# Optimization experiments

Hardware: AMD Instinct MI355X
Metric: run time of the kernel (lower is better)

Reference implementation:

```python
import jax, jax.numpy as jnp
import numpy as np

N_NODES = 100000
N_EDGES = 50000
NNZ = 800000
C = 256
EPS = 0.0  # fixed (train_eps=False)


def setup_inputs() -> dict:
    key = jax.random.key(0)
    k1, k2, k3, k4, k5 = jax.random.split(key, 5)
    x_0 = jax.random.normal(k1, (N_NODES, C), dtype=jnp.float32)
    node_idx = jax.random.randint(k2, (NNZ,), 0, N_NODES, dtype=jnp.int64 if jax.config.jax_enable_x64 else jnp.int32)
    edge_idx = jax.random.randint(k3, (NNZ,), 0, N_EDGES, dtype=jnp.int64 if jax.config.jax_enable_x64 else jnp.int32)
    W = jax.random.normal(k4, (C, C), dtype=jnp.float32) / np.sqrt(C)
    b = jax.random.normal(k5, (C,), dtype=jnp.float32) * 0.01
    return {"x_0": x_0, "node_idx": node_idx, "edge_idx": edge_idx, "W": W, "b": b}


def reference(x_0, node_idx, edge_idx, W, b):
    # vertex2edge: x_1 = B_1^T @ x_0  (each hyperedge sums its member nodes)
    x_1 = jax.ops.segment_sum(x_0[node_idx], edge_idx, num_segments=N_EDGES)  # (E, C)
    # edge2vertex: m_{1->0} = B_1 @ x_1  (each node sums its incident hyperedges)
    m_1_0 = jax.ops.segment_sum(x_1[edge_idx], node_idx, num_segments=N_NODES)  # (N, C)
    # GIN update: Theta @ ((1+eps) x_0 + m)
    x_0_out = ((1.0 + EPS) * x_0 + m_1_0) @ W.T + b
    # use_norm=False -> no row normalization
    return (x_0_out, x_1)
```

## Files before the change

kernel.cpp:

```cpp
#include <hip/hip_runtime.h>

#define N_NODES 100000
#define N_EDGES 50000
#define NNZ     800000
#define C       256

#define SHC_E 8
#define SHC_N 9
#define NBC_E ((N_EDGES + (1 << SHC_E) - 1) >> SHC_E)
#define NBC_N ((N_NODES + (1 << SHC_N) - 1) >> SHC_N)
#define CHUNK 4096
#define NCHUNK ((NNZ + CHUNK - 1) / CHUNK)

#define CONV_BLOCKS (N_NODES * C / 4 / 256)
#define PREPW_BLOCKS 32

typedef short  bf16x8 __attribute__((ext_vector_type(8)));
typedef float  f32x4  __attribute__((ext_vector_type(4)));

static __device__ __forceinline__ unsigned short f2bf(float f) {
    unsigned int u = __float_as_uint(f);
    u += 0x7FFF + ((u >> 16) & 1);
    return (unsigned short)(u >> 16);
}
static __device__ __forceinline__ float bf2f(unsigned short u) {
    return __uint_as_float(((unsigned int)u) << 16);
}


__global__ void convert_hist(const float* __restrict__ x0, unsigned short* __restrict__ x0b,
                             const int* __restrict__ node_idx, const int* __restrict__ edge_idx,
                             int* __restrict__ gcnt_e, int* __restrict__ gcnt_n,
                             int* __restrict__ chunkhist_e, int* __restrict__ chunkhist_n,
                             const float* __restrict__ W, unsigned short* __restrict__ Wb) {
    int bid = blockIdx.x;
    if (bid < CONV_BLOCKS) {
        size_t i = (size_t)bid * 256 + threadIdx.x;
        float4 v = ((const float4*)x0)[i];
        ushort4 o;
        o.x = f2bf(v.x); o.y = f2bf(v.y); o.z = f2bf(v.z); o.w = f2bf(v.w);
        ((ushort4*)x0b)[i] = o;
    } else if (bid < CONV_BLOCKS + NCHUNK) {
        __shared__ int he[NBC_E], hn[NBC_N];
        const int tid = threadIdx.x;
        const int chunk = bid - CONV_BLOCKS;
        for (int i = tid; i < NBC_E; i += 256) he[i] = 0;
        for (int i = tid; i < NBC_N; i += 256) hn[i] = 0;
        __syncthreads();
        const int start = chunk * CHUNK;
        const int end = (start + CHUNK < NNZ) ? start + CHUNK : NNZ;
        for (int k = start + tid; k < end; k += 256) {
            atomicAdd(&he[edge_idx[k] >> SHC_E], 1);
            atomicAdd(&hn[node_idx[k] >> SHC_N], 1);
        }
        __syncthreads();
        for (int i = tid; i < NBC_E; i += 256) {
            int c = he[i];
            chunkhist_e[chunk * NBC_E + i] = c;
            if (c) atomicAdd(&gcnt_e[i], c);
        }
        for (int i = tid; i < NBC_N; i += 256) {
            int c = hn[i];
            chunkhist_n[chunk * NBC_N + i] = c;
            if (c) atomicAdd(&gcnt_n[i], c);
        }
    } else {
        int idx = (bid - CONV_BLOCKS - NCHUNK) * 256 + threadIdx.x;
        int h = idx >> 12, i = idx & 4095;
        int t = i >> 9, s = (i >> 6) & 7, l = i & 63;
        int m = l & 15, q = l >> 4;
        const float* src = W + (size_t)(h * 128 + 16 * t + m) * C + 32 * s + 8 * q;
        float4 f0 = *(const float4*)(src);
        float4 f1 = *(const float4*)(src + 4);
        unsigned short* d = Wb + (size_t)idx * 8;
        d[0] = f2bf(f0.x); d[1] = f2bf(f0.y); d[2] = f2bf(f0.z); d[3] = f2bf(f0.w);
        d[4] = f2bf(f1.x); d[5] = f2bf(f1.y); d[6] = f2bf(f1.z); d[7] = f2bf(f1.w);
    }
}


__global__ void coarse_scan(const int* __restrict__ gcnt_e, const int* __restrict__ gcnt_n,
                            int* __restrict__ gbase_e, int* __restrict__ gbase_n,
                            int* __restrict__ gcur_e, int* __restrict__ gcur_n) {
    const int* gcnt = (blockIdx.x == 0) ? gcnt_e : gcnt_n;
    int* gbase = (blockIdx.x == 0) ? gbase_e : gbase_n;
    int* gcur  = (blockIdx.x == 0) ? gcur_e : gcur_n;
    const int nb = (blockIdx.x == 0) ? NBC_E : NBC_N;
    int tid = threadIdx.x, lane = tid & 63, wid = tid >> 6;
    int v = (tid < nb) ? gcnt[tid] : 0;
    int incl = v;
#pragma unroll
    for (int s = 1; s < 64; s <<= 1) { int u = __shfl_up(incl, s, 64); if (lane >= s) incl += u; }
    __shared__ int wsum[4];
    if (lane == 63) wsum[wid] = incl;
    __syncthreads();
    int add = 0;
    for (int i = 0; i < wid; i++) add += wsum[i];
    int excl = add + incl - v;
    if (tid <= nb) gbase[tid] = excl;
    if (tid < nb)  gcur[tid]  = excl;
}


__global__ __launch_bounds__(256) void bin_coarse(const int* __restrict__ node_idx,
                                                  const int* __restrict__ edge_idx,
                                                  int* __restrict__ gcur_e, int* __restrict__ gcur_n,
                                                  const int* __restrict__ chunkhist_e,
                                                  const int* __restrict__ chunkhist_n,
                                                  unsigned int* __restrict__ tmp_e,
                                                  unsigned int* __restrict__ tmp_n) {
    __shared__ int hist_e[NBC_E], hist_n[NBC_N];
    __shared__ int base_e[NBC_E], base_n[NBC_N];
    const int tid = threadIdx.x;
    const int chunk = blockIdx.x;
    const int start = chunk * CHUNK;
    const int end = (start + CHUNK < NNZ) ? start + CHUNK : NNZ;

    for (int i = tid; i < NBC_E; i += 256) {
        int c = chunkhist_e[chunk * NBC_E + i];
        base_e[i] = c ? atomicAdd(&gcur_e[i], c) : 0;
        hist_e[i] = 0;
    }
    for (int i = tid; i < NBC_N; i += 256) {
        int c = chunkhist_n[chunk * NBC_N + i];
        base_n[i] = c ? atomicAdd(&gcur_n[i], c) : 0;
        hist_n[i] = 0;
    }
    __syncthreads();

    for (int k = start + tid; k < end; k += 256) {
        int ni = node_idx[k], ei = edge_idx[k];
        int be = ei >> SHC_E;
        int pe = base_e[be] + atomicAdd(&hist_e[be], 1);
        tmp_e[pe] = ((unsigned int)ni << SHC_E) | (unsigned int)(ei & ((1 << SHC_E) - 1));
        int bn = ni >> SHC_N;
        int pn = base_n[bn] + atomicAdd(&hist_n[bn], 1);
        tmp_n[pn] = ((unsigned int)ei << SHC_N) | (unsigned int)(ni & ((1 << SHC_N) - 1));
    }
}


template <int SHC, int NTOT>
static __device__ __forceinline__ void scatter_fine_body(const unsigned int* __restrict__ tmp,
                                                         const int* __restrict__ gbase,
                                                         int* __restrict__ off,
                                                         int* __restrict__ perm,
                                                         int b, int* hist, int* cur, int* wsum) {
    constexpr int NK = 1 << SHC;
    const int tid = threadIdx.x, lane = tid & 63, wid = tid >> 6;
    const int start = gbase[b], end = gbase[b + 1];
    for (int t = tid; t < NK; t += 256) hist[t] = 0;
    __syncthreads();
    for (int k = start + tid; k < end; k += 256)
        atomicAdd(&hist[tmp[k] & (NK - 1)], 1);
    __syncthreads();
    int v0, v1 = 0, local;
    if constexpr (NK == 512) { v0 = hist[2 * tid]; v1 = hist[2 * tid + 1]; local = v0 + v1; }
    else                     { v0 = hist[tid]; local = v0; }
    int incl = local;
#pragma unroll
    for (int s = 1; s < 64; s <<= 1) { int u = __shfl_up(incl, s, 64); if (lane >= s) incl += u; }
    if (lane == 63) wsum[wid] = incl;
    __syncthreads();
    int add = 0;
    for (int i = 0; i < wid; i++) add += wsum[i];
    int base = start + add + incl - local;
    const int kbase = b << SHC;
    if constexpr (NK == 512) {
        int key0 = kbase + 2 * tid;
        if (key0 < NTOT)     off[key0] = base;
        if (key0 + 1 < NTOT) off[key0 + 1] = base + v0;
        cur[2 * tid]     = base;
        cur[2 * tid + 1] = base + v0;
    } else {
        int key0 = kbase + tid;
        if (key0 < NTOT) off[key0] = base;
        cur[tid] = base;
    }
    if (b == ((NTOT - 1) >> SHC) && tid == 0) off[NTOT] = end;
    __syncthreads();
    for (int k = start + tid; k < end; k += 256) {
        unsigned int u = tmp[k];
        int pos = atomicAdd(&cur[u & (NK - 1)], 1);
        perm[pos] = (int)(u >> SHC);
    }
}

__global__ __launch_bounds__(256) void scatter_fine(const unsigned int* __restrict__ tmp_e,
                                                    const unsigned int* __restrict__ tmp_n,
                                                    const int* __restrict__ gbase_e,
                                                    const int* __restrict__ gbase_n,
                                                    int* __restrict__ off_e, int* __restrict__ off_n,
                                                    int* __restrict__ perm_e, int* __restrict__ perm_n) {
    __shared__ int hist[1 << SHC_N], cur[1 << SHC_N], wsum[4];
    if (blockIdx.x < NBC_E)
        scatter_fine_body<SHC_E, N_EDGES>(tmp_e, gbase_e, off_e, perm_e, blockIdx.x, hist, cur, wsum);
    else
        scatter_fine_body<SHC_N, N_NODES>(tmp_n, gbase_n, off_n, perm_n, blockIdx.x - NBC_E, hist, cur, wsum);
}


__global__ void pull_edge(const unsigned short* __restrict__ x0b,
                          const int* __restrict__ off, const int* __restrict__ perm,
                          float* __restrict__ x1, unsigned short* __restrict__ x1b) {
    int e = blockIdx.x * 4 + (threadIdx.x >> 6);
    int lane = threadIdx.x & 63;
    int half = lane >> 5;
    int cl = lane & 31;
    int s0 = off[e], s1 = off[e + 1];
    float a[8] = {0, 0, 0, 0, 0, 0, 0, 0};
    float b[8] = {0, 0, 0, 0, 0, 0, 0, 0};
    int k = s0;
    for (; k + 8 <= s1; k += 8) {
        int r0 = perm[k + half],     r1 = perm[k + 2 + half];
        int r2 = perm[k + 4 + half], r3 = perm[k + 6 + half];
        bf16x8 u0 = *(const bf16x8*)(x0b + (size_t)r0 * C + cl * 8);
        bf16x8 u1 = *(const bf16x8*)(x0b + (size_t)r1 * C + cl * 8);
        bf16x8 u2 = *(const bf16x8*)(x0b + (size_t)r2 * C + cl * 8);
        bf16x8 u3 = *(const bf16x8*)(x0b + (size_t)r3 * C + cl * 8);
#pragma unroll
        for (int j = 0; j < 8; j++) {
            a[j] += bf2f((unsigned short)u0[j]); b[j] += bf2f((unsigned short)u1[j]);
            a[j] += bf2f((unsigned short)u2[j]); b[j] += bf2f((unsigned short)u3[j]);
        }
    }
    for (; k + 2 <= s1; k += 2) {
        int r = perm[k + half];
        bf16x8 u = *(const bf16x8*)(x0b + (size_t)r * C + cl * 8);
#pragma unroll
        for (int j = 0; j < 8; j++) a[j] += bf2f((unsigned short)u[j]);
    }
    if (k < s1 && half == 0) {
        int r = perm[k];
        bf16x8 u = *(const bf16x8*)(x0b + (size_t)r * C + cl * 8);
#pragma unroll
        for (int j = 0; j < 8; j++) a[j] += bf2f((unsigned short)u[j]);
    }
#pragma unroll
    for (int j = 0; j < 8; j++) a[j] += b[j];
#pragma unroll
    for (int j = 0; j < 8; j++) a[j] += __shfl_down(a[j], 32);
    if (half == 0) {
        f32x4 vlo = {a[0], a[1], a[2], a[3]};
        f32x4 vhi = {a[4], a[5], a[6], a[7]};
        __builtin_nontemporal_store(vlo, (f32x4*)(x1 + (size_t)e * C + cl * 8));
        __builtin_nontemporal_store(vhi, (f32x4*)(x1 + (size_t)e * C + cl * 8 + 4));
        bf16x8 o;
#pragma unroll
        for (int j = 0; j < 8; j++) o[j] = (short)f2bf(a[j]);
        *(bf16x8*)(x1b + (size_t)e * C + cl * 8) = o;
    }
}

__global__ void pull_node(const unsigned short* __restrict__ x0b,
                          const unsigned short* __restrict__ x1b,
                          const int* __restrict__ off, const int* __restrict__ perm,
                          unsigned short* __restrict__ xm) {
    int n = blockIdx.x * 4 + (threadIdx.x >> 6);
    int lane = threadIdx.x & 63;
    int half = lane >> 5;
    int cl = lane & 31;
    int s0 = off[n], s1 = off[n + 1];
    float a[8] = {0, 0, 0, 0, 0, 0, 0, 0};
    float b[8] = {0, 0, 0, 0, 0, 0, 0, 0};
    int k = s0;
    for (; k + 8 <= s1; k += 8) {
        int r0 = perm[k + half],     r1 = perm[k + 2 + half];
        int r2 = perm[k + 4 + half], r3 = perm[k + 6 + half];
        bf16x8 u0 = *(const bf16x8*)(x1b + (size_t)r0 * C + cl * 8);
        bf16x8 u1 = *(const bf16x8*)(x1b + (size_t)r1 * C + cl * 8);
        bf16x8 u2 = *(const bf16x8*)(x1b + (size_t)r2 * C + cl * 8);
        bf16x8 u3 = *(const bf16x8*)(x1b + (size_t)r3 * C + cl * 8);
#pragma unroll
        for (int j = 0; j < 8; j++) {
            a[j] += bf2f((unsigned short)u0[j]); b[j] += bf2f((unsigned short)u1[j]);
            a[j] += bf2f((unsigned short)u2[j]); b[j] += bf2f((unsigned short)u3[j]);
        }
    }
    for (; k + 2 <= s1; k += 2) {
        int r = perm[k + half];
        bf16x8 u = *(const bf16x8*)(x1b + (size_t)r * C + cl * 8);
#pragma unroll
        for (int j = 0; j < 8; j++) a[j] += bf2f((unsigned short)u[j]);
    }
    if (k < s1 && half == 0) {
        int r = perm[k];
        bf16x8 u = *(const bf16x8*)(x1b + (size_t)r * C + cl * 8);
#pragma unroll
        for (int j = 0; j < 8; j++) a[j] += bf2f((unsigned short)u[j]);
    }
#pragma unroll
    for (int j = 0; j < 8; j++) a[j] += b[j];
#pragma unroll
    for (int j = 0; j < 8; j++) a[j] += __shfl_down(a[j], 32);
    if (half == 0) {
        bf16x8 xr = *(const bf16x8*)(x0b + (size_t)n * C + cl * 8);
        bf16x8 o;
#pragma unroll
        for (int j = 0; j < 8; j++) o[j] = (short)f2bf(a[j] + bf2f((unsigned short)xr[j]));
        *(bf16x8*)(xm + (size_t)n * C + cl * 8) = o;
    }
}


__global__ __launch_bounds__(512) void mfma_gemm2(const unsigned short* __restrict__ xm,
                                                  const unsigned short* __restrict__ Wb,
                                                  const float* __restrict__ bias,
                                                  float* __restrict__ out) {
    __shared__ unsigned short Bs[8 * 8 * 64 * 8];
    const int rt = blockIdx.x >> 1;
    const int colbase = (blockIdx.x & 1) * 128;
    const int tid = threadIdx.x;

    const unsigned short* wsrc = Wb + (size_t)(blockIdx.x & 1) * (4096 * 8);
#pragma unroll
    for (int it = 0; it < 8; it++) {
        int i = it * 512 + tid;
        *(bf16x8*)(Bs + (size_t)i * 8) = *(const bf16x8*)(wsrc + (size_t)i * 8);
    }

    const int w = tid >> 6, lane = tid & 63;
    const int m = lane & 15, q = lane >> 4;
    const int row = rt * 128 + w * 16 + m;
    const int arow = row < N_NODES ? row : N_NODES - 1;

    bf16x8 a[8];
    const unsigned short* ap = xm + (size_t)arow * C + q * 8;
#pragma unroll
    for (int s = 0; s < 8; s++) a[s] = *(const bf16x8*)(ap + 32 * s);

    __syncthreads();

    f32x4 acc[8];
#pragma unroll
    for (int t = 0; t < 8; t++) acc[t] = (f32x4){0.f, 0.f, 0.f, 0.f};

#pragma unroll
    for (int s = 0; s < 8; s++) {
#pragma unroll
        for (int t = 0; t < 8; t++) {
            bf16x8 b = *(const bf16x8*)(Bs + ((t * 8 + s) * 64 + lane) * 8);
            acc[t] = __builtin_amdgcn_mfma_f32_16x16x32_bf16(a[s], b, acc[t], 0, 0, 0);
        }
    }

    const int r0 = rt * 128 + w * 16 + q * 4;
#pragma unroll
    for (int t = 0; t < 8; t++) {
        float bv = bias[colbase + t * 16 + m];
#pragma unroll
        for (int r = 0; r < 4; r++) {
            int rr = r0 + r;
            if (rr < N_NODES)
                __builtin_nontemporal_store(acc[t][r] + bv,
                                            out + (size_t)rr * C + colbase + t * 16 + m);
        }
    }
}


__global__ void init_kernel(const float* __restrict__ x0, float* __restrict__ out) {
    long long i = (long long)blockIdx.x * blockDim.x + threadIdx.x;
    const long long n_node4 = (long long)N_NODES * C / 4;
    const long long n_tot4  = (long long)(N_NODES + N_EDGES) * C / 4;
    float4* o4 = (float4*)out;
    if (i < n_node4)      o4[i] = ((const float4*)x0)[i];
    else if (i < n_tot4)  o4[i] = make_float4(0.f, 0.f, 0.f, 0.f);
}

__global__ void scatter_add_kernel(const float* __restrict__ src,
                                   const int* __restrict__ src_idx,
                                   const int* __restrict__ dst_idx,
                                   float* __restrict__ dst) {
    int j    = blockIdx.x * (blockDim.x >> 6) + (threadIdx.x >> 6);
    int lane = threadIdx.x & 63;
    if (j >= NNZ) return;
    int s = src_idx[j];
    int d = dst_idx[j];
    const float4 v = *(const float4*)(src + (long long)s * C + lane * 4);
    float* dp = dst + (long long)d * C + lane * 4;
    atomicAdd(dp + 0, v.x); atomicAdd(dp + 1, v.y);
    atomicAdd(dp + 2, v.z); atomicAdd(dp + 3, v.w);
}

__global__ void gin_gemm_kernel(const float* __restrict__ W,
                                const float* __restrict__ b,
                                float* __restrict__ out) {
    int n = blockIdx.x;
    int t = threadIdx.x;
    __shared__ float xs[C];
    float* row = out + (long long)n * C;
    xs[t] = row[t];
    __syncthreads();
    float acc = b[t];
    const float* wrow = W + t * C;
#pragma unroll 8
    for (int k = 0; k < C; k += 4) {
        float4 xv = *(const float4*)(xs + k);
        float4 wv = *(const float4*)(wrow + k);
        acc = fmaf(xv.x, wv.x, acc); acc = fmaf(xv.y, wv.y, acc);
        acc = fmaf(xv.z, wv.z, acc); acc = fmaf(xv.w, wv.w, acc);
    }
    row[t] = acc;
}


extern "C" void kernel_launch(void* const* d_in, const int* in_sizes, int n_in,
                              void* d_out, int out_size, void* d_ws, size_t ws_size,
                              hipStream_t stream) {
    const float* x0       = (const float*)d_in[0];
    const int*   node_idx = (const int*)d_in[1];
    const int*   edge_idx = (const int*)d_in[2];
    const float* W        = (const float*)d_in[3];
    const float* b        = (const float*)d_in[4];
    float* out = (float*)d_out;
    float* x1  = out + (size_t)N_NODES * C;

    char* p = (char*)d_ws;
    size_t used = 0;
    auto alloc = [&](size_t bytes) {
        char* r = p + used;
        used += (bytes + 255) & ~(size_t)255;
        return r;
    };
    int* off_e   = (int*)alloc((N_EDGES + 1) * 4);
    int* off_n   = (int*)alloc((N_NODES + 1) * 4);
    int* gcnt_e  = (int*)alloc(NBC_E * 4);
    int* gcnt_n  = (int*)alloc(NBC_N * 4);
    int* gbase_e = (int*)alloc((NBC_E + 1) * 4);
    int* gbase_n = (int*)alloc((NBC_N + 1) * 4);
    int* gcur_e  = (int*)alloc(NBC_E * 4);
    int* gcur_n  = (int*)alloc(NBC_N * 4);
    int* chunkhist_e = (int*)alloc((size_t)NCHUNK * NBC_E * 4);
    int* chunkhist_n = (int*)alloc((size_t)NCHUNK * NBC_N * 4);
    int* perm_e  = (int*)alloc((size_t)NNZ * 4);
    int* perm_n  = (int*)alloc((size_t)NNZ * 4);
    unsigned short* Wb  = (unsigned short*)alloc((size_t)2 * 4096 * 8 * 2);
    unsigned short* x0b = (unsigned short*)alloc((size_t)N_NODES * C * 2);
    unsigned short* x1b = (unsigned short*)alloc((size_t)N_EDGES * C * 2);
    unsigned short* xm  = (unsigned short*)alloc((size_t)N_NODES * C * 2);

    if (ws_size < used) {
        long long tot4 = (long long)(N_NODES + N_EDGES) * C / 4;
        init_kernel<<<(int)((tot4 + 255) / 256), 256, 0, stream>>>(x0, out);
        int grid = NNZ / 4;
        scatter_add_kernel<<<grid, 256, 0, stream>>>(x0, node_idx, edge_idx, x1);
        scatter_add_kernel<<<grid, 256, 0, stream>>>(x1, edge_idx, node_idx, out);
        gin_gemm_kernel<<<N_NODES, 256, 0, stream>>>(W, b, out);
        return;
    }

    hipMemsetAsync(gcnt_e, 0, (size_t)((char*)gcnt_n - (char*)gcnt_e) + (size_t)NBC_N * 4, stream);

    convert_hist<<<CONV_BLOCKS + NCHUNK + PREPW_BLOCKS, 256, 0, stream>>>(
        x0, x0b, node_idx, edge_idx, gcnt_e, gcnt_n, chunkhist_e, chunkhist_n, W, Wb);

    coarse_scan<<<2, 256, 0, stream>>>(gcnt_e, gcnt_n, gbase_e, gbase_n, gcur_e, gcur_n);

    unsigned int* tmp_e = (unsigned int*)x1b;
    unsigned int* tmp_n = (unsigned int*)xm;
    bin_coarse<<<NCHUNK, 256, 0, stream>>>(node_idx, edge_idx, gcur_e, gcur_n,
                                           chunkhist_e, chunkhist_n, tmp_e, tmp_n);
    scatter_fine<<<NBC_E + NBC_N, 256, 0, stream>>>(tmp_e, tmp_n, gbase_e, gbase_n,
                                                    off_e, off_n, perm_e, perm_n);

    pull_edge<<<N_EDGES / 4, 256, 0, stream>>>(x0b, off_e, perm_e, x1, x1b);
    pull_node<<<N_NODES / 4, 256, 0, stream>>>(x0b, x1b, off_n, perm_n, xm);

    const int row_tiles = (N_NODES + 127) / 128;
    mfma_gemm2<<<row_tiles * 2, 512, 0, stream>>>(xm, Wb, b, out);
}
```

Before: 432.2 us.

## Replace atomic coarse offsets with chunk-prefix sums, unroll edge pull, fuse GEMM column halves

The global atomic bin counters and their memset are removed. coarse_scan now sums the per-chunk histograms directly, and bin_coarse computes each chunk's base offset by summing the histograms of earlier chunks. This makes the binning deterministic and drops a memset, at the cost of O(NCHUNK) serial reads per bin. pull_edge gains a 16-wide unrolled gather loop for more memory-level parallelism. The GEMM now handles both column halves in one block, so each A row tile is loaded once instead of twice, but W is reloaded into LDS each half and the grid is halved.

```diff
diff --git a/kernel.cpp b/kernel.cpp
--- a/kernel.cpp
+++ b/kernel.cpp
@@ -30,7 +30,6 @@
 
 __global__ void convert_hist(const float* __restrict__ x0, unsigned short* __restrict__ x0b,
                              const int* __restrict__ node_idx, const int* __restrict__ edge_idx,
-                             int* __restrict__ gcnt_e, int* __restrict__ gcnt_n,
                              int* __restrict__ chunkhist_e, int* __restrict__ chunkhist_n,
                              const float* __restrict__ W, unsigned short* __restrict__ Wb) {
     int bid = blockIdx.x;
@@ -54,16 +53,8 @@
             atomicAdd(&hn[node_idx[k] >> SHC_N], 1);
         }
         __syncthreads();
-        for (int i = tid; i < NBC_E; i += 256) {
-            int c = he[i];
-            chunkhist_e[chunk * NBC_E + i] = c;
-            if (c) atomicAdd(&gcnt_e[i], c);
-        }
-        for (int i = tid; i < NBC_N; i += 256) {
-            int c = hn[i];
-            chunkhist_n[chunk * NBC_N + i] = c;
-            if (c) atomicAdd(&gcnt_n[i], c);
-        }
+        for (int i = tid; i < NBC_E; i += 256) chunkhist_e[chunk * NBC_E + i] = he[i];
+        for (int i = tid; i < NBC_N; i += 256) chunkhist_n[chunk * NBC_N + i] = hn[i];
     } else {
         int idx = (bid - CONV_BLOCKS - NCHUNK) * 256 + threadIdx.x;
         int h = idx >> 12, i = idx & 4095;
@@ -79,15 +70,15 @@
 }
 
 
-__global__ void coarse_scan(const int* __restrict__ gcnt_e, const int* __restrict__ gcnt_n,
-                            int* __restrict__ gbase_e, int* __restrict__ gbase_n,
-                            int* __restrict__ gcur_e, int* __restrict__ gcur_n) {
-    const int* gcnt = (blockIdx.x == 0) ? gcnt_e : gcnt_n;
+__global__ void coarse_scan(const int* __restrict__ chunkhist_e, const int* __restrict__ chunkhist_n,
+                            int* __restrict__ gbase_e, int* __restrict__ gbase_n) {
+    const int* ch = (blockIdx.x == 0) ? chunkhist_e : chunkhist_n;
     int* gbase = (blockIdx.x == 0) ? gbase_e : gbase_n;
-    int* gcur  = (blockIdx.x == 0) ? gcur_e : gcur_n;
     const int nb = (blockIdx.x == 0) ? NBC_E : NBC_N;
     int tid = threadIdx.x, lane = tid & 63, wid = tid >> 6;
-    int v = (tid < nb) ? gcnt[tid] : 0;
+    int v = 0;
+    if (tid < nb)
+        for (int c = 0; c < NCHUNK; c++) v += ch[c * nb + tid];
     int incl = v;
 #pragma unroll
     for (int s = 1; s < 64; s <<= 1) { int u = __shfl_up(incl, s, 64); if (lane >= s) incl += u; }
@@ -98,13 +89,13 @@
     for (int i = 0; i < wid; i++) add += wsum[i];
     int excl = add + incl - v;
     if (tid <= nb) gbase[tid] = excl;
-    if (tid < nb)  gcur[tid]  = excl;
 }
 
 
 __global__ __launch_bounds__(256) void bin_coarse(const int* __restrict__ node_idx,
                                                   const int* __restrict__ edge_idx,
-                                                  int* __restrict__ gcur_e, int* __restrict__ gcur_n,
+                                                  const int* __restrict__ gbase_e,
+                                                  const int* __restrict__ gbase_n,
                                                   const int* __restrict__ chunkhist_e,
                                                   const int* __restrict__ chunkhist_n,
                                                   unsigned int* __restrict__ tmp_e,
@@ -117,13 +108,15 @@
     const int end = (start + CHUNK < NNZ) ? start + CHUNK : NNZ;
 
     for (int i = tid; i < NBC_E; i += 256) {
-        int c = chunkhist_e[chunk * NBC_E + i];
-        base_e[i] = c ? atomicAdd(&gcur_e[i], c) : 0;
+        int pre = gbase_e[i];
+        for (int c = 0; c < chunk; c++) pre += chunkhist_e[c * NBC_E + i];
+        base_e[i] = pre;
         hist_e[i] = 0;
     }
     for (int i = tid; i < NBC_N; i += 256) {
-        int c = chunkhist_n[chunk * NBC_N + i];
-        base_n[i] = c ? atomicAdd(&gcur_n[i], c) : 0;
+        int pre = gbase_n[i];
+        for (int c = 0; c < chunk; c++) pre += chunkhist_n[c * NBC_N + i];
+        base_n[i] = pre;
         hist_n[i] = 0;
     }
     __syncthreads();
@@ -211,6 +204,27 @@
     float a[8] = {0, 0, 0, 0, 0, 0, 0, 0};
     float b[8] = {0, 0, 0, 0, 0, 0, 0, 0};
     int k = s0;
+    for (; k + 16 <= s1; k += 16) {
+        int r0 = perm[k + half],      r1 = perm[k + 2 + half];
+        int r2 = perm[k + 4 + half],  r3 = perm[k + 6 + half];
+        int r4 = perm[k + 8 + half],  r5 = perm[k + 10 + half];
+        int r6 = perm[k + 12 + half], r7 = perm[k + 14 + half];
+        bf16x8 u0 = *(const bf16x8*)(x0b + (size_t)r0 * C + cl * 8);
+        bf16x8 u1 = *(const bf16x8*)(x0b + (size_t)r1 * C + cl * 8);
+        bf16x8 u2 = *(const bf16x8*)(x0b + (size_t)r2 * C + cl * 8);
+        bf16x8 u3 = *(const bf16x8*)(x0b + (size_t)r3 * C + cl * 8);
+        bf16x8 u4 = *(const bf16x8*)(x0b + (size_t)r4 * C + cl * 8);
+        bf16x8 u5 = *(const bf16x8*)(x0b + (size_t)r5 * C + cl * 8);
+        bf16x8 u6 = *(const bf16x8*)(x0b + (size_t)r6 * C + cl * 8);
+        bf16x8 u7 = *(const bf16x8*)(x0b + (size_t)r7 * C + cl * 8);
+#pragma unroll
+        for (int j = 0; j < 8; j++) {
+            a[j] += bf2f((unsigned short)u0[j]); b[j] += bf2f((unsigned short)u1[j]);
+            a[j] += bf2f((unsigned short)u2[j]); b[j] += bf2f((unsigned short)u3[j]);
+            a[j] += bf2f((unsigned short)u4[j]); b[j] += bf2f((unsigned short)u5[j]);
+            a[j] += bf2f((unsigned short)u6[j]); b[j] += bf2f((unsigned short)u7[j]);
+        }
+    }
     for (; k + 8 <= s1; k += 8) {
         int r0 = perm[k + half],     r1 = perm[k + 2 + half];
         int r2 = perm[k + 4 + half], r3 = perm[k + 6 + half];
@@ -303,22 +317,13 @@
 }
 
 
-__global__ __launch_bounds__(512) void mfma_gemm2(const unsigned short* __restrict__ xm,
+__global__ __launch_bounds__(512) void mfma_gemm3(const unsigned short* __restrict__ xm,
                                                   const unsigned short* __restrict__ Wb,
                                                   const float* __restrict__ bias,
                                                   float* __restrict__ out) {
-    __shared__ unsigned short Bs[8 * 8 * 64 * 8];
-    const int rt = blockIdx.x >> 1;
-    const int colbase = (blockIdx.x & 1) * 128;
+    __shared__ unsigned short Bs[4096 * 8];
+    const int rt = blockIdx.x;
     const int tid = threadIdx.x;
-
-    const unsigned short* wsrc = Wb + (size_t)(blockIdx.x & 1) * (4096 * 8);
-#pragma unroll
-    for (int it = 0; it < 8; it++) {
-        int i = it * 512 + tid;
-        *(bf16x8*)(Bs + (size_t)i * 8) = *(const bf16x8*)(wsrc + (size_t)i * 8);
-    }
-
     const int w = tid >> 6, lane = tid & 63;
     const int m = lane & 15, q = lane >> 4;
     const int row = rt * 128 + w * 16 + m;
@@ -329,31 +334,41 @@
 #pragma unroll
     for (int s = 0; s < 8; s++) a[s] = *(const bf16x8*)(ap + 32 * s);
 
-    __syncthreads();
-
-    f32x4 acc[8];
-#pragma unroll
-    for (int t = 0; t < 8; t++) acc[t] = (f32x4){0.f, 0.f, 0.f, 0.f};
-
-#pragma unroll
-    for (int s = 0; s < 8; s++) {
+    const int r0 = rt * 128 + w * 16 + q * 4;
+
+    for (int h = 0; h < 2; h++) {
+        __syncthreads();
+        const unsigned short* wsrc = Wb + (size_t)h * (4096 * 8);
+#pragma unroll
+        for (int it = 0; it < 8; it++) {
+            int i = it * 512 + tid;
+            *(bf16x8*)(Bs + (size_t)i * 8) = *(const bf16x8*)(wsrc + (size_t)i * 8);
+        }
+        __syncthreads();
+
+        f32x4 acc[8];
+#pragma unroll
+        for (int t = 0; t < 8; t++) acc[t] = (f32x4){0.f, 0.f, 0.f, 0.f};
+#pragma unroll
+        for (int s = 0; s < 8; s++) {
+#pragma unroll
+            for (int t = 0; t < 8; t++) {
+                bf16x8 b = *(const bf16x8*)(Bs + ((t * 8 + s) * 64 + lane) * 8);
+                acc[t] = __builtin_amdgcn_mfma_f32_16x16x32_bf16(a[s], b, acc[t], 0, 0, 0);
+            }
+        }
+
+        const int colbase = h * 128;
 #pragma unroll
         for (int t = 0; t < 8; t++) {
-            bf16x8 b = *(const bf16x8*)(Bs + ((t * 8 + s) * 64 + lane) * 8);
-            acc[t] = __builtin_amdgcn_mfma_f32_16x16x32_bf16(a[s], b, acc[t], 0, 0, 0);
-        }
-    }
-
-    const int r0 = rt * 128 + w * 16 + q * 4;
-#pragma unroll
-    for (int t = 0; t < 8; t++) {
-        float bv = bias[colbase + t * 16 + m];
-#pragma unroll
-        for (int r = 0; r < 4; r++) {
-            int rr = r0 + r;
-            if (rr < N_NODES)
-                __builtin_nontemporal_store(acc[t][r] + bv,
-                                            out + (size_t)rr * C + colbase + t * 16 + m);
+            float bv = bias[colbase + t * 16 + m];
+#pragma unroll
+            for (int r = 0; r < 4; r++) {
+                int rr = r0 + r;
+                if (rr < N_NODES)
+                    __builtin_nontemporal_store(acc[t][r] + bv,
+                                                out + (size_t)rr * C + colbase + t * 16 + m);
+            }
         }
     }
 }
@@ -425,12 +440,8 @@
     };
     int* off_e   = (int*)alloc((N_EDGES + 1) * 4);
     int* off_n   = (int*)alloc((N_NODES + 1) * 4);
-    int* gcnt_e  = (int*)alloc(NBC_E * 4);
-    int* gcnt_n  = (int*)alloc(NBC_N * 4);
     int* gbase_e = (int*)alloc((NBC_E + 1) * 4);
     int* gbase_n = (int*)alloc((NBC_N + 1) * 4);
-    int* gcur_e  = (int*)alloc(NBC_E * 4);
-    int* gcur_n  = (int*)alloc(NBC_N * 4);
     int* chunkhist_e = (int*)alloc((size_t)NCHUNK * NBC_E * 4);
     int* chunkhist_n = (int*)alloc((size_t)NCHUNK * NBC_N * 4);
     int* perm_e  = (int*)alloc((size_t)NNZ * 4);
@@ -450,16 +461,14 @@
         return;
     }
 
-    hipMemsetAsync(gcnt_e, 0, (size_t)((char*)gcnt_n - (char*)gcnt_e) + (size_t)NBC_N * 4, stream);
-
     convert_hist<<<CONV_BLOCKS + NCHUNK + PREPW_BLOCKS, 256, 0, stream>>>(
-        x0, x0b, node_idx, edge_idx, gcnt_e, gcnt_n, chunkhist_e, chunkhist_n, W, Wb);
-
-    coarse_scan<<<2, 256, 0, stream>>>(gcnt_e, gcnt_n, gbase_e, gbase_n, gcur_e, gcur_n);
+        x0, x0b, node_idx, edge_idx, chunkhist_e, chunkhist_n, W, Wb);
+
+    coarse_scan<<<2, 256, 0, stream>>>(chunkhist_e, chunkhist_n, gbase_e, gbase_n);
 
     unsigned int* tmp_e = (unsigned int*)x1b;
     unsigned int* tmp_n = (unsigned int*)xm;
-    bin_coarse<<<NCHUNK, 256, 0, stream>>>(node_idx, edge_idx, gcur_e, gcur_n,
+    bin_coarse<<<NCHUNK, 256, 0, stream>>>(node_idx, edge_idx, gbase_e, gbase_n,
                                            chunkhist_e, chunkhist_n, tmp_e, tmp_n);
     scatter_fine<<<NBC_E + NBC_N, 256, 0, stream>>>(tmp_e, tmp_n, gbase_e, gbase_n,
                                                     off_e, off_n, perm_e, perm_n);
@@ -468,5 +477,5 @@
     pull_node<<<N_NODES / 4, 256, 0, stream>>>(x0b, x1b, off_n, perm_n, xm);
 
     const int row_tiles = (N_NODES + 127) / 128;
-    mfma_gemm2<<<row_tiles * 2, 512, 0, stream>>>(xm, Wb, b, out);
-}
+    mfma_gemm3<<<row_tiles, 512, 0, stream>>>(xm, Wb, b, out);
+}
```

After: 480.6 us. +11.2%, slower.
